# Optimization experiments

Hardware: AMD Instinct MI355X
Metric: run time of the kernel (lower is better)

Reference implementation:

```python
import jax, jax.numpy as jnp
import numpy as np

N = 50000      # nodes
E = 800000     # edges (avg degree 16)
F_IN = 512
HID = 128
OUT = 64
NIDX = 1000


def setup_inputs() -> dict:
    key = jax.random.key(0)
    ks = jax.random.split(key, 7)
    x = jax.random.normal(ks[0], (N, F_IN), dtype=jnp.float32)
    edge_src = jax.random.randint(ks[1], (E,), 0, N)
    edge_dst = jax.random.randint(ks[2], (E,), 0, N)
    edge_weight = jax.random.uniform(ks[3], (E,), dtype=jnp.float32)
    W0 = jax.random.normal(ks[4], (F_IN, HID), dtype=jnp.float32) * (1.0 / np.sqrt(F_IN))
    W1 = jax.random.normal(ks[5], (HID, OUT), dtype=jnp.float32) * (1.0 / np.sqrt(HID))
    idx = jax.random.randint(ks[6], (NIDX,), 0, N)
    return {"x": x, "W0": W0, "W1": W1, "edge_weight": edge_weight,
            "edge_src": edge_src, "edge_dst": edge_dst, "idx": idx}


def _spmm(edge_src, edge_dst, edge_weight, h):
    # sparse adj @ h in COO form: gather rows by src, weight, scatter-add to dst
    msg = h[edge_src] * edge_weight[:, None]          # [E, d]
    return jax.ops.segment_sum(msg, edge_dst, num_segments=N)  # [N, d]


def reference(x, W0, W1, edge_weight, edge_src, edge_dst, idx):
    # layer 0: GraphConvolution (x @ W then adj spmm), relu; dropout omitted (eval)
    h = jax.nn.relu(_spmm(edge_src, edge_dst, edge_weight, x @ W0))  # [N, HID]
    # layer 1: final GraphConvolution, no activation
    out = _spmm(edge_src, edge_dst, edge_weight, h @ W1)             # [N, OUT]
    return out[idx]                                                  # [NIDX, OUT]
```

## Files before the change

kernel.cpp:

```cpp
#include <hip/hip_runtime.h>
#include <hip/hip_bf16.h>

#define N_NODES 50000
#define F_IN    512
#define HID     128
#define OUT_F   64
#define NIDX    1000
#define E_NUM   800000
#define CAP     48
#define MAXFLAG 20480
#define NSCAN   196
#define NGBLK   782

typedef __attribute__((ext_vector_type(8))) short short8;
typedef __attribute__((ext_vector_type(4))) float f32x4;

__device__ inline ushort f2bf(float f) {
    __hip_bfloat16 h = __float2bfloat16(f);
    return *reinterpret_cast<ushort*>(&h);
}
__device__ inline float bf2f(ushort u) {
    return __uint_as_float(((uint)u) << 16);
}
__device__ inline short8 pack8(f32x4 a, f32x4 b) {
    short8 r;
    r[0] = (short)f2bf(a[0]); r[1] = (short)f2bf(a[1]);
    r[2] = (short)f2bf(a[2]); r[3] = (short)f2bf(a[3]);
    r[4] = (short)f2bf(b[0]); r[5] = (short)f2bf(b[1]);
    r[6] = (short)f2bf(b[2]); r[7] = (short)f2bf(b[3]);
    return r;
}

#define GLOAD_LDS16(g, l) __builtin_amdgcn_global_load_lds( \
    (const __attribute__((address_space(1))) unsigned int*)(g), \
    (__attribute__((address_space(3))) unsigned int*)(l), 16, 0, 0)

__global__ __launch_bounds__(256) void prep_kernel(const float* __restrict__ W0,
                                                   ushort* __restrict__ W0t,
                                                   const int* __restrict__ idx,
                                                   ushort* __restrict__ jmap) {
    const int b = blockIdx.x;
    if (b < 64) {
        __shared__ float tl[32][33];
        const int k0 = (b & 15) * 32, n0 = (b >> 4) * 32;
        const int tx = threadIdx.x & 31, ty = threadIdx.x >> 5;
#pragma unroll
        for (int i = 0; i < 4; ++i)
            tl[ty + i * 8][tx] = W0[(size_t)(k0 + ty + i * 8) * HID + n0 + tx];
        __syncthreads();
#pragma unroll
        for (int i = 0; i < 4; ++i) {
            const int n = ty + i * 8;
            W0t[(size_t)(n0 + n) * F_IN + k0 + tx] = f2bf(tl[tx][n]);
        }
    } else {
        const int j = (b - 64) * 256 + threadIdx.x;
        if (j < NIDX) jmap[idx[j]] = (ushort)(j + 1);
    }
}

__global__ __launch_bounds__(256, 5) void fused_gemm_scan2(
        const float* __restrict__ x, const ushort* __restrict__ W0t,
        ushort* __restrict__ XW0b,
        const int* __restrict__ esrc, const int* __restrict__ edst,
        const float* __restrict__ ew, const ushort* __restrict__ flags,
        int* __restrict__ countsB, int2* __restrict__ bktB) {
    __shared__ __align__(16) char smem[32768];

    if (blockIdx.x < NSCAN) {
        for (int q = blockIdx.x * 256 + threadIdx.x; q < E_NUM / 4; q += NSCAN * 256) {
            const int e0 = q * 4;
            const int4   d4 = *(const int4*)(edst + e0);
            const int4   s4 = *(const int4*)(esrc + e0);
            const float4 w4 = *(const float4*)(ew + e0);
#define DOIT(DD, SS, WW) { const int s = flags[DD]; if (s) { \
        const int c = atomicAdd(&countsB[s - 1], 1); \
        if (c < CAP) bktB[(size_t)(s - 1) * CAP + c] = make_int2(SS, __float_as_int(WW)); } }
            DOIT(d4.x, s4.x, w4.x) DOIT(d4.y, s4.y, w4.y)
            DOIT(d4.z, s4.z, w4.z) DOIT(d4.w, s4.w, w4.w)
#undef DOIT
        }
        return;
    }

    const int t = threadIdx.x;
    const int w = t >> 6, lane = t & 63;
    const int wr = w >> 1, wc = w & 1;
    const int lr = lane & 15, lk = lane >> 4;
    const int m0 = (blockIdx.x - NSCAN) * 64;

    char* lA = smem;
    char* lB = smem + 16384;
    f32x4 acc[2][4] = {};

    for (int kt = 0; kt < 8; ++kt) {
        const int k0 = kt * 64;
#pragma unroll
        for (int i = 0; i < 4; ++i) {
            const int o = i * 256 + t;
            {
                const int row = o >> 4, c = o & 15;
                int ga = m0 + row; if (ga > N_NODES - 1) ga = N_NODES - 1;
                const float* g = x + (size_t)ga * F_IN + k0 + ((c ^ ((row & 7) << 1)) << 2);
                GLOAD_LDS16(g, lA + (i * 256 + w * 64) * 16);
            }
            {
                const int row = o >> 3, c = o & 7;
                const ushort* g = W0t + (size_t)row * F_IN + k0 + ((c ^ (row & 7)) << 3);
                GLOAD_LDS16(g, lB + (i * 256 + w * 64) * 16);
            }
        }
        __syncthreads();

#pragma unroll
        for (int kk = 0; kk < 2; ++kk) {
            short8 a[2], b[4];
#pragma unroll
            for (int mi = 0; mi < 2; ++mi) {
                const int R = wr * 32 + mi * 16 + lr;
                const int cs = (kk * 8 + lk * 2) ^ ((R & 7) << 1);
                const f32x4 lo = *(const f32x4*)(lA + R * 256 + (cs << 4));
                const f32x4 hi = *(const f32x4*)(lA + R * 256 + (cs << 4) + 16);
                a[mi] = pack8(lo, hi);
            }
#pragma unroll
            for (int ni = 0; ni < 4; ++ni) {
                const int Rb = wc * 64 + ni * 16 + lr;
                const int cs = (kk * 4 + lk) ^ (Rb & 7);
                b[ni] = *(const short8*)(lB + Rb * 128 + (cs << 4));
            }
#pragma unroll
            for (int mi = 0; mi < 2; ++mi)
#pragma unroll
                for (int ni = 0; ni < 4; ++ni)
                    acc[mi][ni] = __builtin_amdgcn_mfma_f32_16x16x32_bf16(
                        a[mi], b[ni], acc[mi][ni], 0, 0, 0);
        }
        __syncthreads();
    }

    float* ep = (float*)smem + w * (16 * 68);
#pragma unroll
    for (int mi = 0; mi < 2; ++mi) {
        __syncthreads();
#pragma unroll
        for (int ni = 0; ni < 4; ++ni)
#pragma unroll
            for (int r = 0; r < 4; ++r)
                ep[(lk * 4 + r) * 68 + ni * 16 + lr] = acc[mi][ni][r];
        __syncthreads();
        const int rr = lane >> 2, cq = lane & 3;
        const int grow = m0 + wr * 32 + mi * 16 + rr;
        alignas(16) float vv[16];
#pragma unroll
        for (int j = 0; j < 4; ++j)
            *(f32x4*)&vv[j * 4] = *(const f32x4*)&ep[rr * 68 + cq * 16 + j * 4];
        if (grow < N_NODES) {
            alignas(16) ushort us[16];
#pragma unroll
            for (int jj = 0; jj < 16; ++jj) us[jj] = f2bf(vv[jj]);
            ushort* orow = XW0b + (size_t)grow * HID + wc * 64 + cq * 16;
            *(uint4*)(orow)     = *(const uint4*)&us[0];
            *(uint4*)(orow + 8) = *(const uint4*)&us[8];
        }
    }
}

__global__ __launch_bounds__(256) void bucket_idx_kernel(const int* __restrict__ esrc,
                                                         const int* __restrict__ edst,
                                                         const float* __restrict__ ew,
                                                         const ushort* __restrict__ jmap,
                                                         int* __restrict__ countsA,
                                                         int2* __restrict__ bktA,
                                                         ushort* __restrict__ flags) {
    const int e0 = (blockIdx.x * 256 + threadIdx.x) * 4;
    if (e0 >= E_NUM) return;
    const int4   d4 = *(const int4*)(edst + e0);
    const int4   s4 = *(const int4*)(esrc + e0);
    const float4 w4 = *(const float4*)(ew + e0);
#define DOIT(DD, SS, WW) { const int rep = jmap[DD]; if (rep) { \
        const int r = rep - 1; const int c = atomicAdd(&countsA[r], 1); \
        if (c < CAP) bktA[(size_t)r * CAP + c] = make_int2(SS, __float_as_int(WW)); \
        flags[SS] = 1; } }
    DOIT(d4.x, s4.x, w4.x) DOIT(d4.y, s4.y, w4.y)
    DOIT(d4.z, s4.z, w4.z) DOIT(d4.w, s4.w, w4.w)
#undef DOIT
}

__global__ __launch_bounds__(256) void compact_kernel(ushort* __restrict__ flags,
                                                      int* __restrict__ list,
                                                      int* __restrict__ nflag) {
    const int n = blockIdx.x * 256 + threadIdx.x;
    if (n < N_NODES && flags[n]) {
        const int s = atomicAdd(nflag, 1);
        if (s < MAXFLAG) { flags[n] = (ushort)(s + 1); list[s] = n; }
        else flags[n] = 0;
    }
}

__global__ __launch_bounds__(256) void spmm1_kernel(const ushort* __restrict__ XW0b,
                                                    const int* __restrict__ list,
                                                    const int* __restrict__ nflag,
                                                    const int* __restrict__ countsB,
                                                    const int2* __restrict__ bktB,
                                                    ushort* __restrict__ H) {
    const int lane = threadIdx.x & 63;
    const int nf = *nflag;
    const int nw = gridDim.x * 4;
    for (int wdx = blockIdx.x * 4 + (threadIdx.x >> 6); wdx < nf; wdx += nw) {
        const int n = list[wdx];
        const int deg = min(countsB[wdx], CAP);
        float a0 = 0.f, a1 = 0.f;
        int c = 0;
        for (; c + 3 < deg; c += 4) {
            const int2 p0 = bktB[(size_t)wdx * CAP + c];
            const int2 p1 = bktB[(size_t)wdx * CAP + c + 1];
            const int2 p2 = bktB[(size_t)wdx * CAP + c + 2];
            const int2 p3 = bktB[(size_t)wdx * CAP + c + 3];
            const uint v0 = *(const uint*)(XW0b + (size_t)p0.x * HID + 2 * lane);
            const uint v1 = *(const uint*)(XW0b + (size_t)p1.x * HID + 2 * lane);
            const uint v2 = *(const uint*)(XW0b + (size_t)p2.x * HID + 2 * lane);
            const uint v3 = *(const uint*)(XW0b + (size_t)p3.x * HID + 2 * lane);
            const float w0 = __int_as_float(p0.y), w1 = __int_as_float(p1.y);
            const float w2 = __int_as_float(p2.y), w3 = __int_as_float(p3.y);
            a0 += w0 * bf2f((ushort)(v0 & 0xffffu)) + w1 * bf2f((ushort)(v1 & 0xffffu))
                + w2 * bf2f((ushort)(v2 & 0xffffu)) + w3 * bf2f((ushort)(v3 & 0xffffu));
            a1 += w0 * bf2f((ushort)(v0 >> 16))     + w1 * bf2f((ushort)(v1 >> 16))
                + w2 * bf2f((ushort)(v2 >> 16))     + w3 * bf2f((ushort)(v3 >> 16));
        }
        for (; c < deg; ++c) {
            const int2 p = bktB[(size_t)wdx * CAP + c];
            const float wt = __int_as_float(p.y);
            const uint v = *(const uint*)(XW0b + (size_t)p.x * HID + 2 * lane);
            a0 += wt * bf2f((ushort)(v & 0xffffu));
            a1 += wt * bf2f((ushort)(v >> 16));
        }
        const uint o = (uint)f2bf(fmaxf(a0, 0.f)) | ((uint)f2bf(fmaxf(a1, 0.f)) << 16);
        *(uint*)(H + (size_t)n * HID + 2 * lane) = o;
    }
}

__global__ __launch_bounds__(64) void spmm2_kernel(const ushort* __restrict__ H,
                                                   const float* __restrict__ W1,
                                                   const int* __restrict__ idx,
                                                   const ushort* __restrict__ jmap,
                                                   const int* __restrict__ countsA,
                                                   const int2* __restrict__ bktA,
                                                   float* __restrict__ outp) {
    __shared__ float aggs[HID];
    const int j = blockIdx.x, lane = threadIdx.x;
    const int r = (int)jmap[idx[j]] - 1;
    const int deg = min(countsA[r], CAP);
    float a0 = 0.f, a1 = 0.f;
    for (int c = 0; c < deg; ++c) {
        const int2 p = bktA[(size_t)r * CAP + c];
        const float wt = __int_as_float(p.y);
        const uint v = *(const uint*)(H + (size_t)p.x * HID + 2 * lane);
        a0 += wt * bf2f((ushort)(v & 0xffffu));
        a1 += wt * bf2f((ushort)(v >> 16));
    }
    aggs[2 * lane] = a0; aggs[2 * lane + 1] = a1;
    __syncthreads();
    float s = 0.f;
#pragma unroll 8
    for (int k = 0; k < HID; ++k) s += aggs[k] * W1[k * OUT_F + lane];
    outp[(size_t)j * OUT_F + lane] = s;
}

extern "C" void kernel_launch(void* const* d_in, const int* in_sizes, int n_in,
                              void* d_out, int out_size, void* d_ws, size_t ws_size,
                              hipStream_t stream) {
    const float* x    = (const float*)d_in[0];
    const float* W0   = (const float*)d_in[1];
    const float* W1   = (const float*)d_in[2];
    const float* ew   = (const float*)d_in[3];
    const int*   esrc = (const int*)d_in[4];
    const int*   edst = (const int*)d_in[5];
    const int*   idx  = (const int*)d_in[6];
    float* outp = (float*)d_out;

    char* ws = (char*)d_ws;
    ushort* XW0b   = (ushort*)(ws);
    ushort* H      = (ushort*)(ws + 12800000);
    ushort* W0t    = (ushort*)(ws + 25600000);
    int2*   bktA   = (int2*)  (ws + 25731072);
    int2*   bktB   = (int2*)  (ws + 26115072);
    int*    list   = (int*)   (ws + 33979392);
    char*   zbase  = ws + 34061312;
    int*    countsA = (int*)   (zbase);
    int*    countsB = (int*)   (zbase + 4096);
    ushort* flags   = (ushort*)(zbase + 86016);
    ushort* jmap    = (ushort*)(zbase + 186368);
    int*    nflag   = (int*)   (zbase + 286720);
    hipMemsetAsync(zbase, 0, 286976, stream);

    prep_kernel      <<<68, 256, 0, stream>>>(W0, W0t, idx, jmap);
    bucket_idx_kernel<<<(E_NUM / 4 + 255) / 256, 256, 0, stream>>>(esrc, edst, ew, jmap, countsA, bktA, flags);
    compact_kernel   <<<(N_NODES + 255) / 256, 256, 0, stream>>>(flags, list, nflag);
    fused_gemm_scan2 <<<NSCAN + NGBLK, 256, 0, stream>>>(
                         x, W0t, XW0b, esrc, edst, ew, flags, countsB, bktB);
    spmm1_kernel     <<<1024, 256, 0, stream>>>(XW0b, list, nflag, countsB, bktB, H);
    spmm2_kernel     <<<NIDX, 64, 0, stream>>>(H, W1, idx, jmap, countsA, bktA, outp);
}
```

Baseline: 91.74 us.

## Index layer-1 buckets by node id and drop the compaction kernel

Removes compact_kernel and the compacted node list. Layer-1 edge buckets and counts are now addressed directly by destination node id, and spmm1 walks every node and skips those without a flag. The scan blocks of the fused GEMM/scan kernel move to the end of the grid and their count rises from 196 to 768. This saves a launch and a serialization point, at the cost of a much larger bucket array, a larger memset and a flag check on all nodes in spmm1.

New measurement: 92.24 us. No clear change (+0.5%).

```diff
diff --git a/kernel.cpp b/kernel.cpp
--- a/kernel.cpp
+++ b/kernel.cpp
@@ -8,9 +8,8 @@
 #define NIDX    1000
 #define E_NUM   800000
 #define CAP     48
-#define MAXFLAG 20480
-#define NSCAN   196
-#define NGBLK   782
+#define NGB     782
+#define NSCAN2  768
 
 typedef __attribute__((ext_vector_type(8))) short short8;
 typedef __attribute__((ext_vector_type(4))) float f32x4;
@@ -56,113 +55,6 @@
     } else {
         const int j = (b - 64) * 256 + threadIdx.x;
         if (j < NIDX) jmap[idx[j]] = (ushort)(j + 1);
-    }
-}
-
-__global__ __launch_bounds__(256, 5) void fused_gemm_scan2(
-        const float* __restrict__ x, const ushort* __restrict__ W0t,
-        ushort* __restrict__ XW0b,
-        const int* __restrict__ esrc, const int* __restrict__ edst,
-        const float* __restrict__ ew, const ushort* __restrict__ flags,
-        int* __restrict__ countsB, int2* __restrict__ bktB) {
-    __shared__ __align__(16) char smem[32768];
-
-    if (blockIdx.x < NSCAN) {
-        for (int q = blockIdx.x * 256 + threadIdx.x; q < E_NUM / 4; q += NSCAN * 256) {
-            const int e0 = q * 4;
-            const int4   d4 = *(const int4*)(edst + e0);
-            const int4   s4 = *(const int4*)(esrc + e0);
-            const float4 w4 = *(const float4*)(ew + e0);
-#define DOIT(DD, SS, WW) { const int s = flags[DD]; if (s) { \
-        const int c = atomicAdd(&countsB[s - 1], 1); \
-        if (c < CAP) bktB[(size_t)(s - 1) * CAP + c] = make_int2(SS, __float_as_int(WW)); } }
-            DOIT(d4.x, s4.x, w4.x) DOIT(d4.y, s4.y, w4.y)
-            DOIT(d4.z, s4.z, w4.z) DOIT(d4.w, s4.w, w4.w)
-#undef DOIT
-        }
-        return;
-    }
-
-    const int t = threadIdx.x;
-    const int w = t >> 6, lane = t & 63;
-    const int wr = w >> 1, wc = w & 1;
-    const int lr = lane & 15, lk = lane >> 4;
-    const int m0 = (blockIdx.x - NSCAN) * 64;
-
-    char* lA = smem;
-    char* lB = smem + 16384;
-    f32x4 acc[2][4] = {};
-
-    for (int kt = 0; kt < 8; ++kt) {
-        const int k0 = kt * 64;
-#pragma unroll
-        for (int i = 0; i < 4; ++i) {
-            const int o = i * 256 + t;
-            {
-                const int row = o >> 4, c = o & 15;
-                int ga = m0 + row; if (ga > N_NODES - 1) ga = N_NODES - 1;
-                const float* g = x + (size_t)ga * F_IN + k0 + ((c ^ ((row & 7) << 1)) << 2);
-                GLOAD_LDS16(g, lA + (i * 256 + w * 64) * 16);
-            }
-            {
-                const int row = o >> 3, c = o & 7;
-                const ushort* g = W0t + (size_t)row * F_IN + k0 + ((c ^ (row & 7)) << 3);
-                GLOAD_LDS16(g, lB + (i * 256 + w * 64) * 16);
-            }
-        }
-        __syncthreads();
-
-#pragma unroll
-        for (int kk = 0; kk < 2; ++kk) {
-            short8 a[2], b[4];
-#pragma unroll
-            for (int mi = 0; mi < 2; ++mi) {
-                const int R = wr * 32 + mi * 16 + lr;
-                const int cs = (kk * 8 + lk * 2) ^ ((R & 7) << 1);
-                const f32x4 lo = *(const f32x4*)(lA + R * 256 + (cs << 4));
-                const f32x4 hi = *(const f32x4*)(lA + R * 256 + (cs << 4) + 16);
-                a[mi] = pack8(lo, hi);
-            }
-#pragma unroll
-            for (int ni = 0; ni < 4; ++ni) {
-                const int Rb = wc * 64 + ni * 16 + lr;
-                const int cs = (kk * 4 + lk) ^ (Rb & 7);
-                b[ni] = *(const short8*)(lB + Rb * 128 + (cs << 4));
-            }
-#pragma unroll
-            for (int mi = 0; mi < 2; ++mi)
-#pragma unroll
-                for (int ni = 0; ni < 4; ++ni)
-                    acc[mi][ni] = __builtin_amdgcn_mfma_f32_16x16x32_bf16(
-                        a[mi], b[ni], acc[mi][ni], 0, 0, 0);
-        }
-        __syncthreads();
-    }
-
-    float* ep = (float*)smem + w * (16 * 68);
-#pragma unroll
-    for (int mi = 0; mi < 2; ++mi) {
-        __syncthreads();
-#pragma unroll
-        for (int ni = 0; ni < 4; ++ni)
-#pragma unroll
-            for (int r = 0; r < 4; ++r)
-                ep[(lk * 4 + r) * 68 + ni * 16 + lr] = acc[mi][ni][r];
-        __syncthreads();
-        const int rr = lane >> 2, cq = lane & 3;
-        const int grow = m0 + wr * 32 + mi * 16 + rr;
-        alignas(16) float vv[16];
-#pragma unroll
-        for (int j = 0; j < 4; ++j)
-            *(f32x4*)&vv[j * 4] = *(const f32x4*)&ep[rr * 68 + cq * 16 + j * 4];
-        if (grow < N_NODES) {
-            alignas(16) ushort us[16];
-#pragma unroll
-            for (int jj = 0; jj < 16; ++jj) us[jj] = f2bf(vv[jj]);
-            ushort* orow = XW0b + (size_t)grow * HID + wc * 64 + cq * 16;
-            *(uint4*)(orow)     = *(const uint4*)&us[0];
-            *(uint4*)(orow + 8) = *(const uint4*)&us[8];
-        }
     }
 }
 
@@ -187,36 +79,129 @@
 #undef DOIT
 }
 
-__global__ __launch_bounds__(256) void compact_kernel(ushort* __restrict__ flags,
-                                                      int* __restrict__ list,
-                                                      int* __restrict__ nflag) {
-    const int n = blockIdx.x * 256 + threadIdx.x;
-    if (n < N_NODES && flags[n]) {
-        const int s = atomicAdd(nflag, 1);
-        if (s < MAXFLAG) { flags[n] = (ushort)(s + 1); list[s] = n; }
-        else flags[n] = 0;
+__global__ __launch_bounds__(256, 5) void fused_gemm_scan2(
+        const float* __restrict__ x, const ushort* __restrict__ W0t,
+        ushort* __restrict__ XW0b,
+        const int* __restrict__ esrc, const int* __restrict__ edst,
+        const float* __restrict__ ew, const ushort* __restrict__ flags,
+        int* __restrict__ countsB, int2* __restrict__ bktB) {
+    __shared__ __align__(16) char smem[32768];
+
+    if (blockIdx.x >= NGB) {
+        for (int q = (blockIdx.x - NGB) * 256 + threadIdx.x; q < E_NUM / 4;
+             q += NSCAN2 * 256) {
+            const int e0 = q * 4;
+            const int4   d4 = *(const int4*)(edst + e0);
+            const int4   s4 = *(const int4*)(esrc + e0);
+            const float4 w4 = *(const float4*)(ew + e0);
+#define DO2(DD, SS, WW) { if (flags[DD]) { \
+        const int c = atomicAdd(&countsB[DD], 1); \
+        if (c < CAP) bktB[(size_t)(DD) * CAP + c] = make_int2(SS, __float_as_int(WW)); } }
+            DO2(d4.x, s4.x, w4.x) DO2(d4.y, s4.y, w4.y)
+            DO2(d4.z, s4.z, w4.z) DO2(d4.w, s4.w, w4.w)
+#undef DO2
+        }
+        return;
+    }
+
+    const int t = threadIdx.x;
+    const int w = t >> 6, lane = t & 63;
+    const int wr = w >> 1, wc = w & 1;
+    const int lr = lane & 15, lk = lane >> 4;
+    const int m0 = blockIdx.x * 64;
+
+    char* lA = smem;
+    char* lB = smem + 16384;
+    f32x4 acc[2][4] = {};
+
+    for (int kt = 0; kt < 8; ++kt) {
+        const int k0 = kt * 64;
+#pragma unroll
+        for (int i = 0; i < 4; ++i) {
+            const int o = i * 256 + t;
+            {
+                const int row = o >> 4, c = o & 15;
+                int ga = m0 + row; if (ga > N_NODES - 1) ga = N_NODES - 1;
+                const float* g = x + (size_t)ga * F_IN + k0 + ((c ^ ((row & 7) << 1)) << 2);
+                GLOAD_LDS16(g, lA + (i * 256 + w * 64) * 16);
+            }
+            {
+                const int row = o >> 3, c = o & 7;
+                const ushort* g = W0t + (size_t)row * F_IN + k0 + ((c ^ (row & 7)) << 3);
+                GLOAD_LDS16(g, lB + (i * 256 + w * 64) * 16);
+            }
+        }
+        __syncthreads();
+
+#pragma unroll
+        for (int kk = 0; kk < 2; ++kk) {
+            short8 a[2], b[4];
+#pragma unroll
+            for (int mi = 0; mi < 2; ++mi) {
+                const int R = wr * 32 + mi * 16 + lr;
+                const int cs = (kk * 8 + lk * 2) ^ ((R & 7) << 1);
+                const f32x4 lo = *(const f32x4*)(lA + R * 256 + (cs << 4));
+                const f32x4 hi = *(const f32x4*)(lA + R * 256 + (cs << 4) + 16);
+                a[mi] = pack8(lo, hi);
+            }
+#pragma unroll
+            for (int ni = 0; ni < 4; ++ni) {
+                const int Rb = wc * 64 + ni * 16 + lr;
+                const int cs = (kk * 4 + lk) ^ (Rb & 7);
+                b[ni] = *(const short8*)(lB + Rb * 128 + (cs << 4));
+            }
+#pragma unroll
+            for (int mi = 0; mi < 2; ++mi)
+#pragma unroll
+                for (int ni = 0; ni < 4; ++ni)
+                    acc[mi][ni] = __builtin_amdgcn_mfma_f32_16x16x32_bf16(
+                        a[mi], b[ni], acc[mi][ni], 0, 0, 0);
+        }
+        __syncthreads();
+    }
+
+    float* ep = (float*)smem + w * (16 * 68);
+#pragma unroll
+    for (int mi = 0; mi < 2; ++mi) {
+        __syncthreads();
+#pragma unroll
+        for (int ni = 0; ni < 4; ++ni)
+#pragma unroll
+            for (int r = 0; r < 4; ++r)
+                ep[(lk * 4 + r) * 68 + ni * 16 + lr] = acc[mi][ni][r];
+        __syncthreads();
+        const int rr = lane >> 2, cq = lane & 3;
+        const int grow = m0 + wr * 32 + mi * 16 + rr;
+        alignas(16) float vv[16];
+#pragma unroll
+        for (int j = 0; j < 4; ++j)
+            *(f32x4*)&vv[j * 4] = *(const f32x4*)&ep[rr * 68 + cq * 16 + j * 4];
+        if (grow < N_NODES) {
+            alignas(16) ushort us[16];
+#pragma unroll
+            for (int jj = 0; jj < 16; ++jj) us[jj] = f2bf(vv[jj]);
+            ushort* orow = XW0b + (size_t)grow * HID + wc * 64 + cq * 16;
+            *(uint4*)(orow)     = *(const uint4*)&us[0];
+            *(uint4*)(orow + 8) = *(const uint4*)&us[8];
+        }
     }
 }
 
 __global__ __launch_bounds__(256) void spmm1_kernel(const ushort* __restrict__ XW0b,
-                                                    const int* __restrict__ list,
-                                                    const int* __restrict__ nflag,
+                                                    const ushort* __restrict__ flags,
                                                     const int* __restrict__ countsB,
                                                     const int2* __restrict__ bktB,
                                                     ushort* __restrict__ H) {
-    const int lane = threadIdx.x & 63;
-    const int nf = *nflag;
-    const int nw = gridDim.x * 4;
-    for (int wdx = blockIdx.x * 4 + (threadIdx.x >> 6); wdx < nf; wdx += nw) {
-        const int n = list[wdx];
-        const int deg = min(countsB[wdx], CAP);
+    const int wv = threadIdx.x >> 6, lane = threadIdx.x & 63;
+    for (int n = blockIdx.x * 4 + wv; n < N_NODES; n += gridDim.x * 4) {
+        if (!flags[n]) continue;
+        const int deg = min(countsB[n], CAP);
+        const int2* brow = bktB + (size_t)n * CAP;
         float a0 = 0.f, a1 = 0.f;
         int c = 0;
         for (; c + 3 < deg; c += 4) {
-            const int2 p0 = bktB[(size_t)wdx * CAP + c];
-            const int2 p1 = bktB[(size_t)wdx * CAP + c + 1];
-            const int2 p2 = bktB[(size_t)wdx * CAP + c + 2];
-            const int2 p3 = bktB[(size_t)wdx * CAP + c + 3];
+            const int2 p0 = brow[c],     p1 = brow[c + 1];
+            const int2 p2 = brow[c + 2], p3 = brow[c + 3];
             const uint v0 = *(const uint*)(XW0b + (size_t)p0.x * HID + 2 * lane);
             const uint v1 = *(const uint*)(XW0b + (size_t)p1.x * HID + 2 * lane);
             const uint v2 = *(const uint*)(XW0b + (size_t)p2.x * HID + 2 * lane);
@@ -229,7 +214,7 @@
                 + w2 * bf2f((ushort)(v2 >> 16))     + w3 * bf2f((ushort)(v3 >> 16));
         }
         for (; c < deg; ++c) {
-            const int2 p = bktB[(size_t)wdx * CAP + c];
+            const int2 p = brow[c];
             const float wt = __int_as_float(p.y);
             const uint v = *(const uint*)(XW0b + (size_t)p.x * HID + 2 * lane);
             a0 += wt * bf2f((ushort)(v & 0xffffu));
@@ -285,20 +270,17 @@
     ushort* W0t    = (ushort*)(ws + 25600000);
     int2*   bktA   = (int2*)  (ws + 25731072);
     int2*   bktB   = (int2*)  (ws + 26115072);
-    int*    list   = (int*)   (ws + 33979392);
-    char*   zbase  = ws + 34061312;
+    char*   zbase  = ws + 45315072;
     int*    countsA = (int*)   (zbase);
     int*    countsB = (int*)   (zbase + 4096);
-    ushort* flags   = (ushort*)(zbase + 86016);
-    ushort* jmap    = (ushort*)(zbase + 186368);
-    int*    nflag   = (int*)   (zbase + 286720);
-    hipMemsetAsync(zbase, 0, 286976, stream);
+    ushort* flags   = (ushort*)(zbase + 208896);
+    ushort* jmap    = (ushort*)(zbase + 309248);
+    hipMemsetAsync(zbase, 0, 409600, stream);
 
     prep_kernel      <<<68, 256, 0, stream>>>(W0, W0t, idx, jmap);
     bucket_idx_kernel<<<(E_NUM / 4 + 255) / 256, 256, 0, stream>>>(esrc, edst, ew, jmap, countsA, bktA, flags);
-    compact_kernel   <<<(N_NODES + 255) / 256, 256, 0, stream>>>(flags, list, nflag);
-    fused_gemm_scan2 <<<NSCAN + NGBLK, 256, 0, stream>>>(
+    fused_gemm_scan2 <<<NGB + NSCAN2, 256, 0, stream>>>(
                          x, W0t, XW0b, esrc, edst, ew, flags, countsB, bktB);
-    spmm1_kernel     <<<1024, 256, 0, stream>>>(XW0b, list, nflag, countsB, bktB, H);
+    spmm1_kernel     <<<1024, 256, 0, stream>>>(XW0b, flags, countsB, bktB, H);
     spmm2_kernel     <<<NIDX, 64, 0, stream>>>(H, W1, idx, jmap, countsA, bktA, outp);
 }
```
